# Kernel optimization log

Hardware: AMD Instinct MI355X
Metric: run time of the kernel (lower is better)

## Reference

```python
import jax, jax.numpy as jnp
import numpy as np

N_NODES = 32_000
N_EDGES = 512_000
D_NODE_IN = 3
D_EDGE_IN = 3
LATENT = 32
HIDDEN = 128
MP_ITERS = 4
D_OUT = 1


def _w(key, shape):
    # fan-in scaled init (lecun-normal-ish), fan_in is the second-to-last dim
    return jax.random.normal(key, shape, jnp.float32) / jnp.sqrt(jnp.float32(shape[-2]))


def _mlp(x, w0, w1, w2):
    # MLP with nb_layers=2 hidden relu layers + linear output, no biases
    return jax.nn.relu(jax.nn.relu(x @ w0) @ w1) @ w2


def setup_inputs() -> dict:
    key = jax.random.key(0)
    ks = jax.random.split(key, 32)
    inp = {
        "input_node": jax.random.normal(ks[0], (N_NODES, D_NODE_IN), jnp.float32),
        "input_edge": jax.random.normal(ks[1], (N_EDGES, D_EDGE_IN), jnp.float32),
        "graph_index": jax.random.randint(ks[2], (N_EDGES, 2), 0, N_NODES, jnp.int32),
        # node encoder: D_NODE_IN -> H -> H -> LATENT
        "enc_n_w0": _w(ks[3], (D_NODE_IN, HIDDEN)),
        "enc_n_w1": _w(ks[4], (HIDDEN, HIDDEN)),
        "enc_n_w2": _w(ks[5], (HIDDEN, LATENT)),
        # edge encoder: D_EDGE_IN -> H -> H -> LATENT
        "enc_e_w0": _w(ks[6], (D_EDGE_IN, HIDDEN)),
        "enc_e_w1": _w(ks[7], (HIDDEN, HIDDEN)),
        "enc_e_w2": _w(ks[8], (HIDDEN, LATENT)),
        # per-iteration edge processor MLP: 3*LATENT -> H -> H -> LATENT (stacked over MP_ITERS)
        "ep_w0": _w(ks[9], (MP_ITERS, 3 * LATENT, HIDDEN)),
        "ep_w1": _w(ks[10], (MP_ITERS, HIDDEN, HIDDEN)),
        "ep_w2": _w(ks[11], (MP_ITERS, HIDDEN, LATENT)),
        # per-iteration node processor MLP: 2*LATENT -> H -> H -> LATENT
        "np_w0": _w(ks[12], (MP_ITERS, 2 * LATENT, HIDDEN)),
        "np_w1": _w(ks[13], (MP_ITERS, HIDDEN, HIDDEN)),
        "np_w2": _w(ks[14], (MP_ITERS, HIDDEN, LATENT)),
        # node decoder: LATENT -> H -> H -> D_OUT
        "dec_w0": _w(ks[15], (LATENT, HIDDEN)),
        "dec_w1": _w(ks[16], (HIDDEN, HIDDEN)),
        "dec_w2": _w(ks[17], (HIDDEN, D_OUT)),
    }
    return inp


def reference(input_node, input_edge, graph_index,
              enc_n_w0, enc_n_w1, enc_n_w2,
              enc_e_w0, enc_e_w1, enc_e_w2,
              ep_w0, ep_w1, ep_w2,
              np_w0, np_w1, np_w2,
              dec_w0, dec_w1, dec_w2):
    senders = graph_index[:, 0]
    receivers = graph_index[:, 1]
    n_nodes = input_node.shape[0]

    node = _mlp(input_node, enc_n_w0, enc_n_w1, enc_n_w2)  # [N, LATENT]
    edge = _mlp(input_edge, enc_e_w0, enc_e_w1, enc_e_w2)  # [E, LATENT]

    def step(carry, ws):
        node, edge = carry
        ew0, ew1, ew2, nw0, nw1, nw2 = ws
        # edge update: concat(edge, node[sender], node[receiver]) -> MLP -> residual
        e_in = jnp.concatenate([edge, node[senders], node[receivers]], axis=-1)
        edge = _mlp(e_in, ew0, ew1, ew2) + edge
        # jraph aggregates edges to nodes; NodeProcessor uses only received aggregation
        recv_agg = jax.ops.segment_sum(edge, receivers, num_segments=n_nodes)
        n_in = jnp.concatenate([node, recv_agg], axis=-1)
        node = _mlp(n_in, nw0, nw1, nw2) + node
        return (node, edge), None

    (node, edge), _ = jax.lax.scan(
        step, (node, edge), (ep_w0, ep_w1, ep_w2, np_w0, np_w1, np_w2))

    return _mlp(node, dec_w0, dec_w1, dec_w2)  # [N, D_OUT]
```

## Files before the change

### kernel.cpp

```cpp
#include <hip/hip_runtime.h>

typedef __attribute__((ext_vector_type(8))) _Float16 f16x8;
typedef __attribute__((ext_vector_type(4))) _Float16 f16x4;
typedef __attribute__((ext_vector_type(4))) float f32x4;

#define DI __device__ __forceinline__
#define BAR() asm volatile("s_waitcnt lgkmcnt(0)\n\ts_barrier" ::: "memory")

DI f32x4 mfma16(f16x8 a, f16x8 b, f32x4 c) {
    return __builtin_amdgcn_mfma_f32_16x16x32_f16(a, b, c, 0, 0, 0);
}


template <int NK>
DI void load_wf2(const _Float16* __restrict__ wt, int Kp, int nbase, int l16, int q,
                 f16x8 f[NK][2]) {
#pragma unroll
    for (int nt = 0; nt < 2; ++nt) {
        int n = nbase + nt * 16 + l16;
#pragma unroll
        for (int ks = 0; ks < NK; ++ks)
            f[ks][nt] = *(const f16x8*)(wt + n * Kp + ks * 32 + q * 8);
    }
}

template <int NK0, int MH>
DI void l01(const f16x8 (*w0f)[2], const f16x8 (*w1f)[2],
            const _Float16* __restrict__ X, int xstride,
            _Float16* __restrict__ H0, _Float16* __restrict__ H1,
            int l16, int w, int q) {
    const f32x4 zero = {0.f, 0.f, 0.f, 0.f};
    f32x4 acc[2][MH];
#pragma unroll
    for (int nt = 0; nt < 2; ++nt)
#pragma unroll
        for (int mt = 0; mt < MH; ++mt) acc[nt][mt] = zero;
#pragma unroll
    for (int ks = 0; ks < NK0; ++ks) {
        f16x8 x[MH];
#pragma unroll
        for (int mt = 0; mt < MH; ++mt)
            x[mt] = *(const f16x8*)(X + (mt * 16 + l16) * xstride + ks * 32 + q * 8);
#pragma unroll
        for (int nt = 0; nt < 2; ++nt)
#pragma unroll
            for (int mt = 0; mt < MH; ++mt)
                acc[nt][mt] = mfma16(w0f[ks][nt], x[mt], acc[nt][mt]);
    }
#pragma unroll
    for (int mt = 0; mt < MH; ++mt)
#pragma unroll
        for (int nt = 0; nt < 2; ++nt) {
            f16x4 h;
#pragma unroll
            for (int i = 0; i < 4; ++i) h[i] = (_Float16)fmaxf(acc[nt][mt][i], 0.f);
            *(f16x4*)(H0 + (mt * 16 + l16) * 136 + w * 32 + nt * 16 + q * 4) = h;
        }
    BAR();
    f32x4 a1[2][MH];
#pragma unroll
    for (int nt = 0; nt < 2; ++nt)
#pragma unroll
        for (int mt = 0; mt < MH; ++mt) a1[nt][mt] = zero;
#pragma unroll
    for (int ks = 0; ks < 4; ++ks) {
        f16x8 x[MH];
#pragma unroll
        for (int mt = 0; mt < MH; ++mt)
            x[mt] = *(const f16x8*)(H0 + (mt * 16 + l16) * 136 + ks * 32 + q * 8);
#pragma unroll
        for (int nt = 0; nt < 2; ++nt)
#pragma unroll
            for (int mt = 0; mt < MH; ++mt)
                a1[nt][mt] = mfma16(w1f[ks][nt], x[mt], a1[nt][mt]);
    }
#pragma unroll
    for (int mt = 0; mt < MH; ++mt)
#pragma unroll
        for (int nt = 0; nt < 2; ++nt) {
            f16x4 h;
#pragma unroll
            for (int i = 0; i < 4; ++i) h[i] = (_Float16)fmaxf(a1[nt][mt][i], 0.f);
            *(f16x4*)(H1 + (mt * 16 + l16) * 136 + w * 32 + nt * 16 + q * 4) = h;
        }
    BAR();
}

DI f32x4 l2g(const f16x8* w2f, const _Float16* __restrict__ H1, int l16, int w,
             int q, int g) {
    int m = (w >> 1) * 16 + l16 + 32 * g;
    f32x4 acc = {0.f, 0.f, 0.f, 0.f};
#pragma unroll
    for (int ks = 0; ks < 4; ++ks) {
        f16x8 x = *(const f16x8*)(H1 + m * 136 + ks * 32 + q * 8);
        acc = mfma16(w2f[ks], x, acc);
    }
    return acc;
}

struct WPtrs { const float* p[15]; };

__global__ void k_prep(WPtrs wp, _Float16* __restrict__ ws) {
    int b = blockIdx.x;
    const float* src; int K, N, Np, Kp, off;
    if (b == 0)       { src = wp.p[0];  K = 3;   N = 128; Np = 128; Kp = 32;  off = 0; }
    else if (b == 1)  { src = wp.p[1];  K = 128; N = 128; Np = 128; Kp = 128; off = 4096; }
    else if (b == 2)  { src = wp.p[2];  K = 128; N = 32;  Np = 32;  Kp = 128; off = 20480; }
    else if (b == 3)  { src = wp.p[3];  K = 3;   N = 128; Np = 128; Kp = 32;  off = 24576; }
    else if (b == 4)  { src = wp.p[4];  K = 128; N = 128; Np = 128; Kp = 128; off = 28672; }
    else if (b == 5)  { src = wp.p[5];  K = 128; N = 32;  Np = 32;  Kp = 128; off = 45056; }
    else if (b <= 9)  { int t = b - 6;  src = wp.p[6] + t * 12288;  K = 96;  N = 128; Np = 128; Kp = 96;  off = 49152 + t * 32768; }
    else if (b <= 13) { int t = b - 10; src = wp.p[7] + t * 16384;  K = 128; N = 128; Np = 128; Kp = 128; off = 61440 + t * 32768; }
    else if (b <= 17) { int t = b - 14; src = wp.p[8] + t * 4096;   K = 128; N = 32;  Np = 32;  Kp = 128; off = 77824 + t * 32768; }
    else if (b <= 21) { int t = b - 18; src = wp.p[9] + t * 8192;   K = 64;  N = 128; Np = 128; Kp = 64;  off = 180224 + t * 28672; }
    else if (b <= 25) { int t = b - 22; src = wp.p[10] + t * 16384; K = 128; N = 128; Np = 128; Kp = 128; off = 188416 + t * 28672; }
    else if (b <= 29) { int t = b - 26; src = wp.p[11] + t * 4096;  K = 128; N = 32;  Np = 32;  Kp = 128; off = 204800 + t * 28672; }
    else if (b == 30) { src = wp.p[12]; K = 32;  N = 128; Np = 128; Kp = 32;  off = 294912; }
    else if (b == 31) { src = wp.p[13]; K = 128; N = 128; Np = 128; Kp = 128; off = 299008; }
    else              { src = wp.p[14]; K = 128; N = 1;   Np = 16;  Kp = 128; off = 315392; }
    int total = Np * Kp;
    for (int i = threadIdx.x; i < total; i += 256) {
        int n = i / Kp, k = i - n * Kp;
        float v = (k < K && n < N) ? src[k * N + n] : 0.f;
        ws[off + i] = (_Float16)v;
    }
}

__global__ void k_zero(unsigned* __restrict__ p, int n) {
    int i = blockIdx.x * 256 + threadIdx.x;
    if (i < n) p[i] = 0u;
}
__global__ void k_hist(const int* __restrict__ gi, unsigned* __restrict__ cnt) {
    int e = blockIdx.x * 256 + threadIdx.x;
    if (e < 512000) atomicAdd(&cnt[gi[2 * e + 1]], 1u);
}
__global__ __launch_bounds__(1024) void k_scan(
    const unsigned* __restrict__ cnt, unsigned* __restrict__ rowptr,
    unsigned* __restrict__ cursor) {
    __shared__ unsigned s[1024];
    int t = threadIdx.x;
    unsigned loc[32];
    unsigned sum = 0;
#pragma unroll
    for (int i = 0; i < 32; ++i) {
        int idx = t * 32 + i;
        unsigned v = (idx < 32000) ? cnt[idx] : 0u;
        loc[i] = v; sum += v;
    }
    s[t] = sum;
    __syncthreads();
#pragma unroll
    for (int d = 1; d < 1024; d <<= 1) {
        unsigned x = (t >= d) ? s[t - d] : 0u;
        __syncthreads();
        s[t] += x;
        __syncthreads();
    }
    if (t == 1023) rowptr[32000] = s[1023];
    unsigned off = (t == 0) ? 0u : s[t - 1];
#pragma unroll
    for (int i = 0; i < 32; ++i) {
        int idx = t * 32 + i;
        if (idx < 32000) { rowptr[idx] = off; cursor[idx] = off; off += loc[i]; }
    }
}
__global__ void k_scatter(const int* __restrict__ gi, unsigned* __restrict__ cursor,
                          unsigned* __restrict__ iperm, int2* __restrict__ sr) {
    int e = blockIdx.x * 256 + threadIdx.x;
    if (e < 512000) {
        int s = gi[2 * e], r = gi[2 * e + 1];
        unsigned pos = atomicAdd(&cursor[r], 1u);
        iperm[pos] = (unsigned)e;
        sr[pos] = make_int2(s, r);
    }
}

__global__ __launch_bounds__(256, 3) void k_enc(
    const float* __restrict__ in, _Float16* __restrict__ out,
    const _Float16* __restrict__ w0t, const _Float16* __restrict__ w1t,
    const _Float16* __restrict__ w2t, int NT, const unsigned* __restrict__ iperm) {
    __shared__ __align__(16) _Float16 Xp[64 * 40];
    __shared__ __align__(16) _Float16 H0[64 * 136];
    __shared__ __align__(16) _Float16 H1[64 * 136];
    const int tid = threadIdx.x, w = tid >> 6, lane = tid & 63;
    const int q = lane >> 4, l16 = lane & 15;
    f16x8 w0f[1][2], w1f[4][2], w2f[4];
    load_wf2<1>(w0t, 32, w * 32, l16, q, w0f);
    load_wf2<4>(w1t, 128, w * 32, l16, q, w1f);
    {
        int n2 = (w & 1) * 16 + l16;
#pragma unroll
        for (int ks = 0; ks < 4; ++ks)
            w2f[ks] = *(const f16x8*)(w2t + n2 * 128 + ks * 32 + q * 8);
    }
    for (int c = tid; c < 2560; c += 256) Xp[c] = (_Float16)0.f;
    BAR();

    const int g = gridDim.x;
    const int dr = tid / 3, dc = tid - dr * 3;
    const int orow = (w >> 1) * 16 + l16, ocol = (w & 1) * 16 + q * 4;
    int t = blockIdx.x;

    while (true) {
        if (tid < 192) {
            unsigned e = iperm ? iperm[t * 64 + dr] : (unsigned)(t * 64 + dr);
            Xp[dr * 40 + dc] = (_Float16)in[e * 3 + dc];
        }
        BAR();
        l01<1, 4>(w0f, w1f, Xp, 40, H0, H1, l16, w, q);
#pragma unroll
        for (int gg = 0; gg < 2; ++gg) {
            f32x4 o = l2g(w2f, H1, l16, w, q, gg);
            f16x4 ov;
#pragma unroll
            for (int i = 0; i < 4; ++i) ov[i] = (_Float16)o[i];
            *(f16x4*)(out + (t * 64 + gg * 32 + orow) * 32 + ocol) = ov;
        }
        t += g;
        if (t >= NT) break;
    }
}

__global__ __launch_bounds__(256, 3) void k_edge(
    const _Float16* __restrict__ node, _Float16* __restrict__ edgeP,
    const int2* __restrict__ sr,
    const _Float16* __restrict__ w0t, const _Float16* __restrict__ w1t,
    const _Float16* __restrict__ w2t) {
    __shared__ __align__(16) _Float16 Xe[64 * 104];
    __shared__ __align__(16) _Float16 H0[64 * 136];
    __shared__ __align__(16) _Float16 H1[64 * 136];
    const int tid = threadIdx.x, w = tid >> 6, lane = tid & 63;
    const int q = lane >> 4, l16 = lane & 15;
    f16x8 w0f[3][2], w1f[4][2], w2f[4];
    load_wf2<3>(w0t, 96, w * 32, l16, q, w0f);
    load_wf2<4>(w1t, 128, w * 32, l16, q, w1f);
    {
        int n2 = (w & 1) * 16 + l16;
#pragma unroll
        for (int ks = 0; ks < 4; ++ks)
            w2f[ks] = *(const f16x8*)(w2t + n2 * 128 + ks * 32 + q * 8);
    }
    int cr[3], cs[3];
#pragma unroll
    for (int j = 0; j < 3; ++j) {
        int c = tid + 256 * j;
        cr[j] = c / 12; cs[j] = c - cr[j] * 12;
    }
    const int orow = (w >> 1) * 16 + l16, ocol = (w & 1) * 16 + q * 4;

    const int NT = 8000, g = gridDim.x;
    int t = blockIdx.x;
    int2 srv[3];
#pragma unroll
    for (int j = 0; j < 3; ++j) srv[j] = sr[t * 64 + cr[j]];

    while (true) {
        int tn = t + g; if (tn >= NT) tn = t;
        int4 v[3];
#pragma unroll
        for (int j = 0; j < 3; ++j) {
            int s = cs[j];
            const _Float16* src = (s < 4) ? edgeP + (t * 64 + cr[j]) * 32 + s * 8
                               : (s < 8) ? node + srv[j].x * 32 + (s - 4) * 8
                                         : node + srv[j].y * 32 + (s - 8) * 8;
            v[j] = *(const int4*)src;
        }
        int2 srn[3];
#pragma unroll
        for (int j = 0; j < 3; ++j) srn[j] = sr[tn * 64 + cr[j]];
#pragma unroll
        for (int j = 0; j < 3; ++j)
            *(int4*)(Xe + cr[j] * 104 + cs[j] * 8) = v[j];
        BAR();
        f16x4 oldv[2];
#pragma unroll
        for (int gg = 0; gg < 2; ++gg)
            oldv[gg] = *(const f16x4*)(Xe + (gg * 32 + orow) * 104 + ocol);

        l01<3, 4>(w0f, w1f, Xe, 104, H0, H1, l16, w, q);
#pragma unroll
        for (int gg = 0; gg < 2; ++gg) {
            f32x4 o = l2g(w2f, H1, l16, w, q, gg);
            f16x4 nv;
#pragma unroll
            for (int i = 0; i < 4; ++i) nv[i] = (_Float16)(o[i] + (float)oldv[gg][i]);
            *(f16x4*)(edgeP + (t * 64 + gg * 32 + orow) * 32 + ocol) = nv;
        }

        if (tn == t) break;
        t = tn;
#pragma unroll
        for (int j = 0; j < 3; ++j) srv[j] = srn[j];
    }
}

__global__ __launch_bounds__(256, 3) void k_node(
    _Float16* __restrict__ node, const _Float16* __restrict__ edgeP,
    const unsigned* __restrict__ rowptr,
    const _Float16* __restrict__ w0t, const _Float16* __restrict__ w1t,
    const _Float16* __restrict__ w2t) {
    __shared__ __align__(16) _Float16 Xn[32 * 72];
    __shared__ __align__(16) _Float16 H0[32 * 136];
    __shared__ __align__(16) _Float16 H1[32 * 136];
    const int tid = threadIdx.x, w = tid >> 6, lane = tid & 63;
    const int q = lane >> 4, l16 = lane & 15;
    f16x8 w0f[2][2], w1f[4][2], w2f[4];
    load_wf2<2>(w0t, 64, w * 32, l16, q, w0f);
    load_wf2<4>(w1t, 128, w * 32, l16, q, w1f);
    {
        int n2 = (w & 1) * 16 + l16;
#pragma unroll
        for (int ks = 0; ks < 4; ++ks)
            w2f[ks] = *(const f16x8*)(w2t + n2 * 128 + ks * 32 + q * 8);
    }
    const int t = blockIdx.x;
    const int orow = (w >> 1) * 16 + l16, ocol = (w & 1) * 16 + q * 4;
    {
        int cr = tid >> 3, cs = tid & 7;
        int r = t * 32 + cr;
        if (cs < 4) {
            *(int4*)(Xn + cr * 72 + cs * 8) = *(const int4*)(node + r * 32 + cs * 8);
        } else {
            unsigned b = rowptr[r], e = rowptr[r + 1];
            const _Float16* base = edgeP + (cs - 4) * 8;
            float a0[8], a1[8];
#pragma unroll
            for (int i = 0; i < 8; ++i) { a0[i] = 0.f; a1[i] = 0.f; }
            unsigned p = b;
            for (; p + 2 <= e; p += 2) {
                f16x8 x0 = *(const f16x8*)(base + (p + 0) * 32);
                f16x8 x1 = *(const f16x8*)(base + (p + 1) * 32);
#pragma unroll
                for (int i = 0; i < 8; ++i) { a0[i] += (float)x0[i]; a1[i] += (float)x1[i]; }
            }
            if (p < e) {
                f16x8 x0 = *(const f16x8*)(base + p * 32);
#pragma unroll
                for (int i = 0; i < 8; ++i) a0[i] += (float)x0[i];
            }
            f16x8 h;
#pragma unroll
            for (int i = 0; i < 8; ++i) h[i] = (_Float16)(a0[i] + a1[i]);
            *(f16x8*)(Xn + cr * 72 + cs * 8) = h;
        }
    }
    BAR();
    f16x4 oldv = *(const f16x4*)(Xn + orow * 72 + ocol);
    l01<2, 2>(w0f, w1f, Xn, 72, H0, H1, l16, w, q);
    f32x4 o = l2g(w2f, H1, l16, w, q, 0);
    f16x4 nv;
#pragma unroll
    for (int i = 0; i < 4; ++i) nv[i] = (_Float16)(o[i] + (float)oldv[i]);
    *(f16x4*)(node + (t * 32 + orow) * 32 + ocol) = nv;
}

__global__ __launch_bounds__(256, 3) void k_dec(
    const _Float16* __restrict__ node,
    const _Float16* __restrict__ w0t, const _Float16* __restrict__ w1t,
    const _Float16* __restrict__ w2t, float* __restrict__ out) {
    __shared__ __align__(16) _Float16 Xd[64 * 40];
    __shared__ __align__(16) _Float16 H0[64 * 136];
    __shared__ __align__(16) _Float16 H1[64 * 136];
    const int tid = threadIdx.x, w = tid >> 6, lane = tid & 63;
    const int q = lane >> 4, l16 = lane & 15;
    f16x8 w0f[1][2], w1f[4][2], w2f[4];
    load_wf2<1>(w0t, 32, w * 32, l16, q, w0f);
    load_wf2<4>(w1t, 128, w * 32, l16, q, w1f);
    {
        int n2 = l16;
#pragma unroll
        for (int ks = 0; ks < 4; ++ks)
            w2f[ks] = *(const f16x8*)(w2t + n2 * 128 + ks * 32 + q * 8);
    }
    const int t = blockIdx.x;
    {
        int cr = tid >> 2, cs = tid & 3;
        *(int4*)(Xd + cr * 40 + cs * 8) = *(const int4*)(node + (t * 64 + cr) * 32 + cs * 8);
    }
    BAR();
    l01<1, 4>(w0f, w1f, Xd, 40, H0, H1, l16, w, q);
#pragma unroll
    for (int gg = 0; gg < 2; ++gg) {
        f32x4 o = l2g(w2f, H1, l16, w, q, gg);
        if ((w & 1) == 0 && q == 0) out[t * 64 + gg * 32 + (w >> 1) * 16 + l16] = o[0];
    }
}

extern "C" void kernel_launch(void* const* d_in, const int* in_sizes, int n_in,
                              void* d_out, int out_size, void* d_ws, size_t ws_size,
                              hipStream_t stream) {
    const float* input_node = (const float*)d_in[0];
    const float* input_edge = (const float*)d_in[1];
    const int* gi = (const int*)d_in[2];

    _Float16* ws = (_Float16*)d_ws;
    _Float16* node = (_Float16*)((char*)d_ws + 655360);
    _Float16* edgeP = (_Float16*)((char*)d_ws + 2703360);
    unsigned* rowptr = (unsigned*)((char*)d_ws + 35471360);
    unsigned* cursor = (unsigned*)((char*)d_ws + 35599616);
    unsigned* iperm = (unsigned*)((char*)d_ws + 35727616);
    int2* sr = (int2*)((char*)d_ws + 37775616);

    WPtrs wp;
    for (int i = 0; i < 15; ++i) wp.p[i] = (const float*)d_in[3 + i];

    k_prep<<<33, 256, 0, stream>>>(wp, ws);

    k_zero<<<125, 256, 0, stream>>>(cursor, 32000);
    k_hist<<<2000, 256, 0, stream>>>(gi, cursor);
    k_scan<<<1, 1024, 0, stream>>>(cursor, rowptr, cursor);
    k_scatter<<<2000, 256, 0, stream>>>(gi, cursor, iperm, sr);

    k_enc<<<500, 256, 0, stream>>>(input_node, node, ws + 0, ws + 4096, ws + 20480,
                                   500, nullptr);
    k_enc<<<768, 256, 0, stream>>>(input_edge, edgeP, ws + 24576, ws + 28672,
                                   ws + 45056, 8000, iperm);

    for (int t = 0; t < 4; ++t) {
        k_edge<<<768, 256, 0, stream>>>(node, edgeP, sr,
                                        ws + 49152 + t * 32768,
                                        ws + 61440 + t * 32768,
                                        ws + 77824 + t * 32768);
        k_node<<<1000, 256, 0, stream>>>(node, edgeP, rowptr,
                                         ws + 180224 + t * 28672,
                                         ws + 188416 + t * 28672,
                                         ws + 204800 + t * 28672);
    }
    k_dec<<<500, 256, 0, stream>>>(node, ws + 294912, ws + 299008, ws + 315392,
                                   (float*)d_out);
}
```

Measured before the change: 502.4 us.

## Prefetch next tile's gathered inputs between MLP layers in edge and encoder kernels

Splits the fused layer-0/layer-1 helper into separate l0 and l1 functions. In the edge kernel, the global gathers of the next tile's edge features and sender/receiver node rows are issued between layer 0 and layer 1, so their latency overlaps MFMA work. The encoder loop gets the same treatment for its input reads. This holds extra live registers for the prefetched data, which could hurt occupancy under the 3-blocks-per-CU launch bound. The encoder call also contains an odd always-true null check on w1f.

Measured after the change: 637.0 us. 26.8% more time.

```diff
diff --git a/kernel.cpp b/kernel.cpp
--- a/kernel.cpp
+++ b/kernel.cpp
@@ -25,10 +25,8 @@
 }
 
 template <int NK0, int MH>
-DI void l01(const f16x8 (*w0f)[2], const f16x8 (*w1f)[2],
-            const _Float16* __restrict__ X, int xstride,
-            _Float16* __restrict__ H0, _Float16* __restrict__ H1,
-            int l16, int w, int q) {
+DI void l0(const f16x8 (*w0f)[2], const _Float16* __restrict__ X, int xstride,
+           _Float16* __restrict__ H0, int l16, int w, int q) {
     const f32x4 zero = {0.f, 0.f, 0.f, 0.f};
     f32x4 acc[2][MH];
 #pragma unroll
@@ -57,6 +55,12 @@
             *(f16x4*)(H0 + (mt * 16 + l16) * 136 + w * 32 + nt * 16 + q * 4) = h;
         }
     BAR();
+}
+
+template <int MH>
+DI void l1(const f16x8 (*w1f)[2], const _Float16* __restrict__ H0,
+           _Float16* __restrict__ H1, int l16, int w, int q) {
+    const f32x4 zero = {0.f, 0.f, 0.f, 0.f};
     f32x4 a1[2][MH];
 #pragma unroll
     for (int nt = 0; nt < 2; ++nt)
@@ -201,13 +205,23 @@
     const int orow = (w >> 1) * 16 + l16, ocol = (w & 1) * 16 + q * 4;
     int t = blockIdx.x;
 
+    float val = 0.f;
+    if (tid < 192) {
+        unsigned e = iperm ? iperm[t * 64 + dr] : (unsigned)(t * 64 + dr);
+        val = in[e * 3 + dc];
+    }
+
     while (true) {
+        int tn = t + g; if (tn >= NT) tn = t;
+        if (tid < 192) Xp[dr * 40 + dc] = (_Float16)val;
+        BAR();
+        l0<1, 4>(w0f, w1f == nullptr ? nullptr : Xp, 40, H0, l16, w, q);
+        float valn = 0.f;
         if (tid < 192) {
-            unsigned e = iperm ? iperm[t * 64 + dr] : (unsigned)(t * 64 + dr);
-            Xp[dr * 40 + dc] = (_Float16)in[e * 3 + dc];
-        }
-        BAR();
-        l01<1, 4>(w0f, w1f, Xp, 40, H0, H1, l16, w, q);
+            unsigned en = iperm ? iperm[tn * 64 + dr] : (unsigned)(tn * 64 + dr);
+            valn = in[en * 3 + dc];
+        }
+        l1<4>(w1f, H0, H1, l16, w, q);
 #pragma unroll
         for (int gg = 0; gg < 2; ++gg) {
             f32x4 o = l2g(w2f, H1, l16, w, q, gg);
@@ -216,8 +230,9 @@
             for (int i = 0; i < 4; ++i) ov[i] = (_Float16)o[i];
             *(f16x4*)(out + (t * 64 + gg * 32 + orow) * 32 + ocol) = ov;
         }
-        t += g;
-        if (t >= NT) break;
+        if (tn == t) break;
+        t = tn;
+        val = valn;
     }
 }
 
@@ -250,21 +265,22 @@
 
     const int NT = 8000, g = gridDim.x;
     int t = blockIdx.x;
+
     int2 srv[3];
 #pragma unroll
     for (int j = 0; j < 3; ++j) srv[j] = sr[t * 64 + cr[j]];
+    int4 v[3];
+#pragma unroll
+    for (int j = 0; j < 3; ++j) {
+        int s = cs[j];
+        const _Float16* src = (s < 4) ? edgeP + (t * 64 + cr[j]) * 32 + s * 8
+                           : (s < 8) ? node + srv[j].x * 32 + (s - 4) * 8
+                                     : node + srv[j].y * 32 + (s - 8) * 8;
+        v[j] = *(const int4*)src;
+    }
 
     while (true) {
         int tn = t + g; if (tn >= NT) tn = t;
-        int4 v[3];
-#pragma unroll
-        for (int j = 0; j < 3; ++j) {
-            int s = cs[j];
-            const _Float16* src = (s < 4) ? edgeP + (t * 64 + cr[j]) * 32 + s * 8
-                               : (s < 8) ? node + srv[j].x * 32 + (s - 4) * 8
-                                         : node + srv[j].y * 32 + (s - 8) * 8;
-            v[j] = *(const int4*)src;
-        }
         int2 srn[3];
 #pragma unroll
         for (int j = 0; j < 3; ++j) srn[j] = sr[tn * 64 + cr[j]];
@@ -277,7 +293,17 @@
         for (int gg = 0; gg < 2; ++gg)
             oldv[gg] = *(const f16x4*)(Xe + (gg * 32 + orow) * 104 + ocol);
 
-        l01<3, 4>(w0f, w1f, Xe, 104, H0, H1, l16, w, q);
+        l0<3, 4>(w0f, Xe, 104, H0, l16, w, q);
+        int4 vn[3];
+#pragma unroll
+        for (int j = 0; j < 3; ++j) {
+            int s = cs[j];
+            const _Float16* src = (s < 4) ? edgeP + (tn * 64 + cr[j]) * 32 + s * 8
+                               : (s < 8) ? node + srn[j].x * 32 + (s - 4) * 8
+                                         : node + srn[j].y * 32 + (s - 8) * 8;
+            vn[j] = *(const int4*)src;
+        }
+        l1<4>(w1f, H0, H1, l16, w, q);
 #pragma unroll
         for (int gg = 0; gg < 2; ++gg) {
             f32x4 o = l2g(w2f, H1, l16, w, q, gg);
@@ -290,7 +316,7 @@
         if (tn == t) break;
         t = tn;
 #pragma unroll
-        for (int j = 0; j < 3; ++j) srv[j] = srn[j];
+        for (int j = 0; j < 3; ++j) { v[j] = vn[j]; srv[j] = srn[j]; }
     }
 }
 
@@ -346,7 +372,8 @@
     }
     BAR();
     f16x4 oldv = *(const f16x4*)(Xn + orow * 72 + ocol);
-    l01<2, 2>(w0f, w1f, Xn, 72, H0, H1, l16, w, q);
+    l0<2, 2>(w0f, Xn, 72, H0, l16, w, q);
+    l1<2>(w1f, H0, H1, l16, w, q);
     f32x4 o = l2g(w2f, H1, l16, w, q, 0);
     f16x4 nv;
 #pragma unroll
@@ -378,7 +405,8 @@
         *(int4*)(Xd + cr * 40 + cs * 8) = *(const int4*)(node + (t * 64 + cr) * 32 + cs * 8);
     }
     BAR();
-    l01<1, 4>(w0f, w1f, Xd, 40, H0, H1, l16, w, q);
+    l0<1, 4>(w0f, Xd, 40, H0, l16, w, q);
+    l1<4>(w1f, H0, H1, l16, w, q);
 #pragma unroll
     for (int gg = 0; gg < 2; ++gg) {
         f32x4 o = l2g(w2f, H1, l16, w, q, gg);
```

## Split edge MLP rows across eight waves in 512-thread edge blocks

Applied to the files above, without the earlier changes.

The edge kernel now runs 512 threads per block. Eight waves each compute half the rows (MH=2) of a 64-edge tile, so every wave does less MFMA work and the gather loads are spread over more threads. The l01 helper is split into separate l0/l1 layer helpers that take row and column offsets, and the other kernels are updated to call them. The launch bound now asks for 6 waves per EU, which caps the register budget while each wave still holds the full weight fragments. That risks spills, and each weight fragment is now duplicated across twice as many waves.

Result: slower. 901.2 us (+79.4%).

```diff
diff --git a/kernel.cpp b/kernel.cpp
--- a/kernel.cpp
+++ b/kernel.cpp
@@ -25,10 +25,8 @@
 }
 
 template <int NK0, int MH>
-DI void l01(const f16x8 (*w0f)[2], const f16x8 (*w1f)[2],
-            const _Float16* __restrict__ X, int xstride,
-            _Float16* __restrict__ H0, _Float16* __restrict__ H1,
-            int l16, int w, int q) {
+DI void l0(const f16x8 (*w0f)[2], const _Float16* __restrict__ X, int xstride,
+           _Float16* __restrict__ H0, int l16, int nb, int mb, int q) {
     const f32x4 zero = {0.f, 0.f, 0.f, 0.f};
     f32x4 acc[2][MH];
 #pragma unroll
@@ -40,7 +38,7 @@
         f16x8 x[MH];
 #pragma unroll
         for (int mt = 0; mt < MH; ++mt)
-            x[mt] = *(const f16x8*)(X + (mt * 16 + l16) * xstride + ks * 32 + q * 8);
+            x[mt] = *(const f16x8*)(X + ((mb + mt) * 16 + l16) * xstride + ks * 32 + q * 8);
 #pragma unroll
         for (int nt = 0; nt < 2; ++nt)
 #pragma unroll
@@ -54,9 +52,15 @@
             f16x4 h;
 #pragma unroll
             for (int i = 0; i < 4; ++i) h[i] = (_Float16)fmaxf(acc[nt][mt][i], 0.f);
-            *(f16x4*)(H0 + (mt * 16 + l16) * 136 + w * 32 + nt * 16 + q * 4) = h;
+            *(f16x4*)(H0 + ((mb + mt) * 16 + l16) * 136 + nb + nt * 16 + q * 4) = h;
         }
     BAR();
+}
+
+template <int MH>
+DI void l1(const f16x8 (*w1f)[2], const _Float16* __restrict__ H0,
+           _Float16* __restrict__ H1, int l16, int nb, int mb, int q) {
+    const f32x4 zero = {0.f, 0.f, 0.f, 0.f};
     f32x4 a1[2][MH];
 #pragma unroll
     for (int nt = 0; nt < 2; ++nt)
@@ -67,7 +71,7 @@
         f16x8 x[MH];
 #pragma unroll
         for (int mt = 0; mt < MH; ++mt)
-            x[mt] = *(const f16x8*)(H0 + (mt * 16 + l16) * 136 + ks * 32 + q * 8);
+            x[mt] = *(const f16x8*)(H0 + ((mb + mt) * 16 + l16) * 136 + ks * 32 + q * 8);
 #pragma unroll
         for (int nt = 0; nt < 2; ++nt)
 #pragma unroll
@@ -81,7 +85,7 @@
             f16x4 h;
 #pragma unroll
             for (int i = 0; i < 4; ++i) h[i] = (_Float16)fmaxf(a1[nt][mt][i], 0.f);
-            *(f16x4*)(H1 + (mt * 16 + l16) * 136 + w * 32 + nt * 16 + q * 4) = h;
+            *(f16x4*)(H1 + ((mb + mt) * 16 + l16) * 136 + nb + nt * 16 + q * 4) = h;
         }
     BAR();
 }
@@ -207,7 +211,8 @@
             Xp[dr * 40 + dc] = (_Float16)in[e * 3 + dc];
         }
         BAR();
-        l01<1, 4>(w0f, w1f, Xp, 40, H0, H1, l16, w, q);
+        l0<1, 4>(w0f, Xp, 40, H0, l16, w * 32, 0, q);
+        l1<4>(w1f, H0, H1, l16, w * 32, 0, q);
 #pragma unroll
         for (int gg = 0; gg < 2; ++gg) {
             f32x4 o = l2g(w2f, H1, l16, w, q, gg);
@@ -221,7 +226,7 @@
     }
 }
 
-__global__ __launch_bounds__(256, 3) void k_edge(
+__global__ __launch_bounds__(512, 6) void k_edge(
     const _Float16* __restrict__ node, _Float16* __restrict__ edgeP,
     const int2* __restrict__ sr,
     const _Float16* __restrict__ w0t, const _Float16* __restrict__ w1t,
@@ -231,66 +236,64 @@
     __shared__ __align__(16) _Float16 H1[64 * 136];
     const int tid = threadIdx.x, w = tid >> 6, lane = tid & 63;
     const int q = lane >> 4, l16 = lane & 15;
+    const int w4 = w & 3, mb = (w >> 2) * 2;
     f16x8 w0f[3][2], w1f[4][2], w2f[4];
-    load_wf2<3>(w0t, 96, w * 32, l16, q, w0f);
-    load_wf2<4>(w1t, 128, w * 32, l16, q, w1f);
+    load_wf2<3>(w0t, 96, w4 * 32, l16, q, w0f);
+    load_wf2<4>(w1t, 128, w4 * 32, l16, q, w1f);
     {
         int n2 = (w & 1) * 16 + l16;
 #pragma unroll
         for (int ks = 0; ks < 4; ++ks)
             w2f[ks] = *(const f16x8*)(w2t + n2 * 128 + ks * 32 + q * 8);
     }
-    int cr[3], cs[3];
-#pragma unroll
-    for (int j = 0; j < 3; ++j) {
-        int c = tid + 256 * j;
-        cr[j] = c / 12; cs[j] = c - cr[j] * 12;
-    }
+    const int cr0 = tid / 12, cs0 = tid - cr0 * 12;
+    const int c1 = tid + 512;
+    const int cr1 = c1 / 12, cs1 = c1 - cr1 * 12;
+    const bool has2 = (tid < 256);
     const int orow = (w >> 1) * 16 + l16, ocol = (w & 1) * 16 + q * 4;
 
     const int NT = 8000, g = gridDim.x;
     int t = blockIdx.x;
-    int2 srv[3];
-#pragma unroll
-    for (int j = 0; j < 3; ++j) srv[j] = sr[t * 64 + cr[j]];
+    int2 srv0 = sr[t * 64 + cr0];
+    int2 srv1 = make_int2(0, 0);
+    if (has2) srv1 = sr[t * 64 + cr1];
 
     while (true) {
         int tn = t + g; if (tn >= NT) tn = t;
-        int4 v[3];
-#pragma unroll
-        for (int j = 0; j < 3; ++j) {
-            int s = cs[j];
-            const _Float16* src = (s < 4) ? edgeP + (t * 64 + cr[j]) * 32 + s * 8
-                               : (s < 8) ? node + srv[j].x * 32 + (s - 4) * 8
-                                         : node + srv[j].y * 32 + (s - 8) * 8;
-            v[j] = *(const int4*)src;
-        }
-        int2 srn[3];
-#pragma unroll
-        for (int j = 0; j < 3; ++j) srn[j] = sr[tn * 64 + cr[j]];
-#pragma unroll
-        for (int j = 0; j < 3; ++j)
-            *(int4*)(Xe + cr[j] * 104 + cs[j] * 8) = v[j];
+        int4 v0, v1;
+        {
+            int s = cs0;
+            const _Float16* src = (s < 4) ? edgeP + (t * 64 + cr0) * 32 + s * 8
+                               : (s < 8) ? node + srv0.x * 32 + (s - 4) * 8
+                                         : node + srv0.y * 32 + (s - 8) * 8;
+            v0 = *(const int4*)src;
+        }
+        if (has2) {
+            int s = cs1;
+            const _Float16* src = (s < 4) ? edgeP + (t * 64 + cr1) * 32 + s * 8
+                               : (s < 8) ? node + srv1.x * 32 + (s - 4) * 8
+                                         : node + srv1.y * 32 + (s - 8) * 8;
+            v1 = *(const int4*)src;
+        }
+        int2 srn0 = sr[tn * 64 + cr0];
+        int2 srn1 = make_int2(0, 0);
+        if (has2) srn1 = sr[tn * 64 + cr1];
+        *(int4*)(Xe + cr0 * 104 + cs0 * 8) = v0;
+        if (has2) *(int4*)(Xe + cr1 * 104 + cs1 * 8) = v1;
         BAR();
-        f16x4 oldv[2];
-#pragma unroll
-        for (int gg = 0; gg < 2; ++gg)
-            oldv[gg] = *(const f16x4*)(Xe + (gg * 32 + orow) * 104 + ocol);
-
-        l01<3, 4>(w0f, w1f, Xe, 104, H0, H1, l16, w, q);
-#pragma unroll
-        for (int gg = 0; gg < 2; ++gg) {
-            f32x4 o = l2g(w2f, H1, l16, w, q, gg);
-            f16x4 nv;
-#pragma unroll
-            for (int i = 0; i < 4; ++i) nv[i] = (_Float16)(o[i] + (float)oldv[gg][i]);
-            *(f16x4*)(edgeP + (t * 64 + gg * 32 + orow) * 32 + ocol) = nv;
-        }
+        f16x4 oldv = *(const f16x4*)(Xe + orow * 104 + ocol);
+
+        l0<3, 2>(w0f, Xe, 104, H0, l16, w4 * 32, mb, q);
+        l1<2>(w1f, H0, H1, l16, w4 * 32, mb, q);
+        f32x4 o = l2g(w2f, H1, l16, w, q, 0);
+        f16x4 nv;
+#pragma unroll
+        for (int i = 0; i < 4; ++i) nv[i] = (_Float16)(o[i] + (float)oldv[i]);
+        *(f16x4*)(edgeP + (t * 64 + orow) * 32 + ocol) = nv;
 
         if (tn == t) break;
         t = tn;
-#pragma unroll
-        for (int j = 0; j < 3; ++j) srv[j] = srn[j];
+        srv0 = srn0; srv1 = srn1;
     }
 }
 
@@ -346,7 +349,8 @@
     }
     BAR();
     f16x4 oldv = *(const f16x4*)(Xn + orow * 72 + ocol);
-    l01<2, 2>(w0f, w1f, Xn, 72, H0, H1, l16, w, q);
+    l0<2, 2>(w0f, Xn, 72, H0, l16, w * 32, 0, q);
+    l1<2>(w1f, H0, H1, l16, w * 32, 0, q);
     f32x4 o = l2g(w2f, H1, l16, w, q, 0);
     f16x4 nv;
 #pragma unroll
@@ -378,7 +382,8 @@
         *(int4*)(Xd + cr * 40 + cs * 8) = *(const int4*)(node + (t * 64 + cr) * 32 + cs * 8);
     }
     BAR();
-    l01<1, 4>(w0f, w1f, Xd, 40, H0, H1, l16, w, q);
+    l0<1, 4>(w0f, Xd, 40, H0, l16, w * 32, 0, q);
+    l1<4>(w1f, H0, H1, l16, w * 32, 0, q);
 #pragma unroll
     for (int gg = 0; gg < 2; ++gg) {
         f32x4 o = l2g(w2f, H1, l16, w, q, gg);
@@ -417,7 +422,7 @@
                                    ws + 45056, 8000, iperm);
 
     for (int t = 0; t < 4; ++t) {
-        k_edge<<<768, 256, 0, stream>>>(node, edgeP, sr,
+        k_edge<<<768, 512, 0, stream>>>(node, edgeP, sr,
                                         ws + 49152 + t * 32768,
                                         ws + 61440 + t * 32768,
                                         ws + 77824 + t * 32768);
```
